# Kernel tuning notes

Hardware: AMD Instinct MI355X
Metric: run time of the kernel (lower is better)

## Reference

```python
import jax, jax.numpy as jnp
import numpy as np


def setup_inputs() -> dict:
    key = jax.random.key(0)
    ks = jax.random.split(key, 8)
    B, T, D, S, E, V = 8, 64, 1024, 32, 16, 50257
    SCALE = 0.02  # keep dot-products in a sane range for softmax
    return {
        "decoder_states": jax.random.normal(ks[0], (B, T, D), jnp.float32),
        "scene_memory": jax.random.normal(ks[1], (B, S, D), jnp.float32),
        "embedding_weight": jax.random.normal(ks[2], (V, D), jnp.float32) * SCALE,
        "ent_ids": jax.random.randint(ks[3], (B, S, E), 0, V, jnp.int32),
        "Wq": jax.random.normal(ks[4], (D, D), jnp.float32) * SCALE,
        "bq": jnp.zeros((D,), jnp.float32),
        "Wk": jax.random.normal(ks[5], (D, D), jnp.float32) * SCALE,
        "bk": jnp.zeros((D,), jnp.float32),
        "Wp": jax.random.normal(ks[6], (2 * D, 1), jnp.float32) * SCALE,
        "bp": jnp.full((1,), 3.0, jnp.float32),  # nn.init.constant_(bias, 3.0)
    }


def reference(decoder_states, scene_memory, embedding_weight, ent_ids,
              Wq, bq, Wk, bk, Wp, bp):
    B, T, D = decoder_states.shape
    S = scene_memory.shape[1]
    V = embedding_weight.shape[0]

    # scene-level attention
    q = decoder_states @ Wq + bq            # [B,T,D]
    k = scene_memory @ Wk + bk              # [B,S,D]
    scores = jnp.einsum('btd,bsd->bts', q, k) / jnp.sqrt(jnp.float32(D))
    scene_attn = jax.nn.softmax(scores, axis=-1)          # [B,T,S]
    context = jnp.einsum('bts,bsd->btd', scene_attn, scene_memory)

    # hard p_gen gate
    gate_in = jnp.concatenate([decoder_states, context], axis=-1)  # [B,T,2D]
    p_gen = jax.nn.sigmoid((gate_in @ Wp + bp - 0.5) * 10.0)       # [B,T,1]

    # entity salience per scene, scattered into V-sized tensor
    dec_last = decoder_states[:, -1, :]                   # [B,D]
    ent_embs = embedding_weight[ent_ids]                  # [B,S,E,D] gather
    salience = jax.nn.softmax(
        jnp.einsum('bd,bsed->bse', dec_last, ent_embs), axis=-1)  # [B,S,E]
    bi = jnp.arange(B)[:, None, None]
    si = jnp.arange(S)[None, :, None]
    scene_to_token = jnp.zeros((B, S, V), decoder_states.dtype)
    scene_to_token = scene_to_token.at[bi, si, ent_ids].set(salience)

    pointer_probs = jnp.einsum('bts,bsv->btv', scene_attn, scene_to_token)
    return p_gen, pointer_probs
```

## Files before the change

kernel.cpp:

```cpp
#include <hip/hip_runtime.h>
#include <math.h>

#define BB 8
#define TT 64
#define DD 1024
#define SS 32
#define EE 16
#define VV 50257
#define BT (BB*TT)
#define BS (BB*SS)

__global__ __launch_bounds__(256) void gemm_qk(
    const float* __restrict__ dec, const float* __restrict__ scene,
    const float* __restrict__ Wq, const float* __restrict__ bq,
    const float* __restrict__ Wk, const float* __restrict__ bk,
    float* __restrict__ q, float* __restrict__ k)
{
    __shared__ __align__(16) float As[16][68];
    __shared__ __align__(16) float Bs[16][68];
    const int bn = blockIdx.x;
    const int bm = blockIdx.y;
    const bool isq = (bm < 8);
    const float* X   = isq ? dec : scene;
    const float* W   = isq ? Wq  : Wk;
    const float* bia = isq ? bq  : bk;
    float*       Y   = isq ? q   : k;
    const int row0 = (isq ? bm : bm - 8) * 64;
    const int col0 = bn * 64;
    const int tid = threadIdx.x;
    const int tx = tid & 15, ty = tid >> 4;

    float acc[4][4] = {};
    for (int k0 = 0; k0 < DD; k0 += 16) {
        {
            const int m  = tid >> 2;
            const int kc = (tid & 3) * 4;
            const float4 x4 = *(const float4*)&X[(size_t)(row0 + m) * DD + k0 + kc];
            As[kc + 0][m] = x4.x; As[kc + 1][m] = x4.y;
            As[kc + 2][m] = x4.z; As[kc + 3][m] = x4.w;
        }
        {
            const int kk = tid >> 4;
            const int nc = (tid & 15) * 4;
            *(float4*)&Bs[kk][nc] = *(const float4*)&W[(size_t)(k0 + kk) * DD + col0 + nc];
        }
        __syncthreads();
        #pragma unroll
        for (int kk = 0; kk < 16; ++kk) {
            float a[4], b[4];
            #pragma unroll
            for (int i = 0; i < 4; ++i) a[i] = As[kk][ty * 4 + i];
            #pragma unroll
            for (int j = 0; j < 4; ++j) b[j] = Bs[kk][tx * 4 + j];
            #pragma unroll
            for (int i = 0; i < 4; ++i)
                #pragma unroll
                for (int j = 0; j < 4; ++j)
                    acc[i][j] += a[i] * b[j];
        }
        __syncthreads();
    }
    #pragma unroll
    for (int i = 0; i < 4; ++i) {
        const int r = row0 + ty * 4 + i;
        #pragma unroll
        for (int j = 0; j < 4; ++j) {
            const int c = col0 + tx * 4 + j;
            Y[(size_t)r * DD + c] = acc[i][j] + bia[c];
        }
    }
}

__global__ __launch_bounds__(64) void dots_kernel(
    const float* __restrict__ dec, const float* __restrict__ scene,
    const float* __restrict__ Wp, float* __restrict__ dw, float* __restrict__ mw)
{
    const int b = blockIdx.x;
    const int lane = threadIdx.x;
    const float* x; const float* wp; float* out;
    if (b < BT) { x = dec   + (size_t)b * DD;        wp = Wp;      out = dw + b; }
    else        { x = scene + (size_t)(b - BT) * DD; wp = Wp + DD; out = mw + (b - BT); }
    float s = 0.f;
    #pragma unroll 4
    for (int i = lane; i < DD; i += 64) s += x[i] * wp[i];
    for (int off = 32; off; off >>= 1) s += __shfl_down(s, off);
    if (lane == 0) *out = s;
}

__global__ __launch_bounds__(256) void attn_kernel(
    const float* __restrict__ qm, const float* __restrict__ km,
    const float* __restrict__ dwv, const float* __restrict__ mwv,
    const float* __restrict__ bp,
    float* __restrict__ attn_out, float* __restrict__ pgen_out)
{
    __shared__ __align__(16) float qs[DD];
    __shared__ float sc[SS];
    const int bt = blockIdx.x;
    const int b  = bt / TT;
    const int tid = threadIdx.x;
    for (int i = tid; i < DD; i += 256) qs[i] = qm[(size_t)bt * DD + i];
    __syncthreads();
    const int w = tid >> 6, lane = tid & 63;
    for (int j = 0; j < 8; ++j) {
        const int s = w * 8 + j;
        const float* kr = km + (size_t)(b * SS + s) * DD;
        float acc = 0.f;
        #pragma unroll
        for (int i = 0; i < 16; ++i) acc += qs[lane + 64 * i] * kr[lane + 64 * i];
        for (int off = 32; off; off >>= 1) acc += __shfl_down(acc, off);
        if (lane == 0) sc[s] = acc * 0.03125f;
    }
    __syncthreads();
    if (tid < 64) {
        float v = (lane < SS) ? sc[lane] : -INFINITY;
        float m = v;
        for (int off = 32; off; off >>= 1) m = fmaxf(m, __shfl_xor(m, off));
        float e = (lane < SS) ? __expf(v - m) : 0.f;
        float sum = e;
        for (int off = 32; off; off >>= 1) sum += __shfl_xor(sum, off);
        const float a = e / sum;
        float g = (lane < SS) ? a * mwv[b * SS + lane] : 0.f;
        for (int off = 32; off; off >>= 1) g += __shfl_xor(g, off);
        if (lane < SS) attn_out[bt * SS + lane] = a;
        if (lane == 0) {
            const float z = dwv[bt] + g + bp[0] - 0.5f;
            pgen_out[bt] = 1.0f / (1.0f + __expf(-10.0f * z));
        }
    }
}

__global__ __launch_bounds__(256) void sal_kernel(
    const float* __restrict__ dec, const float* __restrict__ emb,
    const int* __restrict__ ids, float* __restrict__ sal)
{
    __shared__ __align__(16) float ds[DD];
    __shared__ float logit[EE];
    __shared__ int lid[EE];
    const int bs = blockIdx.x;
    const int b  = bs / SS;
    const int tid = threadIdx.x;
    const float* dl = dec + (size_t)(b * TT + (TT - 1)) * DD;
    for (int i = tid; i < DD; i += 256) ds[i] = dl[i];
    if (tid < EE) lid[tid] = ids[bs * EE + tid];
    __syncthreads();
    const int w = tid >> 6, lane = tid & 63;
    for (int j = 0; j < 4; ++j) {
        const int e = w * 4 + j;
        const float* er = emb + (size_t)lid[e] * DD;
        float acc = 0.f;
        #pragma unroll
        for (int i = 0; i < 16; ++i) acc += ds[lane + 64 * i] * er[lane + 64 * i];
        for (int off = 32; off; off >>= 1) acc += __shfl_down(acc, off);
        if (lane == 0) logit[e] = acc;
    }
    __syncthreads();
    if (tid == 0) {
        float m = -INFINITY;
        for (int e = 0; e < EE; ++e) m = fmaxf(m, logit[e]);
        float ex[EE]; float sum = 0.f;
        for (int e = 0; e < EE; ++e) { ex[e] = __expf(logit[e] - m); sum += ex[e]; }
        const float inv = 1.0f / sum;
        for (int e = 0; e < EE; ++e) {
            bool dup = false;
            for (int e2 = e + 1; e2 < EE; ++e2)
                if (lid[e2] == lid[e]) { dup = true; break; }
            sal[bs * EE + e] = dup ? 0.f : ex[e] * inv;
        }
    }
}

__global__ __launch_bounds__(256) void pp_kernel(
    const float* __restrict__ attn, const float* __restrict__ sal,
    const int* __restrict__ ids, float* __restrict__ pp)
{
    __shared__ float at[SS];
    const int bt = blockIdx.x;
    const int b  = bt / TT;
    const int tid = threadIdx.x;
    if (tid < SS) at[tid] = attn[bt * SS + tid];
    float* row = pp + (size_t)bt * VV;
    for (int i = tid; i < VV; i += 256) row[i] = 0.f;
    __syncthreads();
    for (int i = tid; i < SS * EE; i += 256) {
        const int s = i >> 4, e = i & 15;
        const float v = at[s] * sal[(b * SS + s) * EE + e];
        atomicAdd(&row[ids[(b * SS + s) * EE + e]], v);
    }
}

extern "C" void kernel_launch(void* const* d_in, const int* in_sizes, int n_in,
                              void* d_out, int out_size, void* d_ws, size_t ws_size,
                              hipStream_t stream) {
    (void)in_sizes; (void)n_in; (void)ws_size; (void)out_size;
    const float* dec   = (const float*)d_in[0];
    const float* scene = (const float*)d_in[1];
    const float* emb   = (const float*)d_in[2];
    const int*   ids   = (const int*)  d_in[3];
    const float* Wq    = (const float*)d_in[4];
    const float* bq    = (const float*)d_in[5];
    const float* Wk    = (const float*)d_in[6];
    const float* bk    = (const float*)d_in[7];
    const float* Wp    = (const float*)d_in[8];
    const float* bp    = (const float*)d_in[9];
    float* out = (float*)d_out;
    float* ws  = (float*)d_ws;

    float* q    = ws;
    float* k    = q    + 512 * 1024;
    float* attn = k    + 256 * 1024;
    float* sal  = attn + 512 * 32;
    float* dw   = sal  + 256 * 16;
    float* mw   = dw   + 512;

    gemm_qk<<<dim3(16, 12), 256, 0, stream>>>(dec, scene, Wq, bq, Wk, bk, q, k);
    dots_kernel<<<768, 64, 0, stream>>>(dec, scene, Wp, dw, mw);
    attn_kernel<<<512, 256, 0, stream>>>(q, k, dw, mw, bp, attn, out);
    sal_kernel<<<256, 256, 0, stream>>>(dec, emb, ids, sal);
    pp_kernel<<<512, 256, 0, stream>>>(attn, sal, ids, out + 512);
}
```

Baseline: 389.7 us.

## Switch Q/K projection to bf16 MFMA and fuse small kernels

```diff
diff --git a/kernel.cpp b/kernel.cpp
--- a/kernel.cpp
+++ b/kernel.cpp
@@ -1,4 +1,5 @@
 #include <hip/hip_runtime.h>
+#include <hip/hip_bf16.h>
 #include <math.h>
 
 #define BB 8
@@ -10,161 +11,212 @@
 #define BT (BB*TT)
 #define BS (BB*SS)
 
-__global__ __launch_bounds__(256) void gemm_qk(
+typedef __attribute__((ext_vector_type(8))) short short8;
+typedef __attribute__((ext_vector_type(4))) float floatx4;
+
+static __device__ inline unsigned short f2bf(float x) {
+    __hip_bfloat16 h = __float2bfloat16(x);
+    union { __hip_bfloat16 h; unsigned short u; } cv; cv.h = h;
+    return cv.u;
+}
+
+static __device__ inline void gl_lds16(const void* g, void* l) {
+    __builtin_amdgcn_global_load_lds(
+        (const __attribute__((address_space(1))) void*)g,
+        (__attribute__((address_space(3))) void*)l, 16, 0, 0);
+}
+
+__global__ __launch_bounds__(256) void prep_kernel(
     const float* __restrict__ dec, const float* __restrict__ scene,
-    const float* __restrict__ Wq, const float* __restrict__ bq,
-    const float* __restrict__ Wk, const float* __restrict__ bk,
-    float* __restrict__ q, float* __restrict__ k)
-{
-    __shared__ __align__(16) float As[16][68];
-    __shared__ __align__(16) float Bs[16][68];
-    const int bn = blockIdx.x;
-    const int bm = blockIdx.y;
-    const bool isq = (bm < 8);
-    const float* X   = isq ? dec : scene;
-    const float* W   = isq ? Wq  : Wk;
-    const float* bia = isq ? bq  : bk;
-    float*       Y   = isq ? q   : k;
-    const int row0 = (isq ? bm : bm - 8) * 64;
-    const int col0 = bn * 64;
+    const float* __restrict__ Wq, const float* __restrict__ Wk,
+    const float* __restrict__ Wp,
+    unsigned short* __restrict__ Xb, unsigned short* __restrict__ Wt,
+    float* __restrict__ dw, float* __restrict__ mw)
+{
+    __shared__ float tile[64][65];
+    const int bid = blockIdx.x;
+    const int t = threadIdx.x;
+    if (bid < 768) {
+        const int row = bid;
+        const float* src = (row < BT) ? dec + (size_t)row * DD
+                                      : scene + (size_t)(row - BT) * DD;
+        const float4 v = *(const float4*)&src[t * 4];
+        ushort4 u;
+        u.x = f2bf(v.x); u.y = f2bf(v.y); u.z = f2bf(v.z); u.w = f2bf(v.w);
+        *(ushort4*)&Xb[(size_t)row * DD + t * 4] = u;
+    } else if (bid < 1280) {
+        const int tb = bid - 768;
+        const int sel = tb >> 8;
+        const int tt8 = tb & 255;
+        const int k0 = (tt8 >> 4) * 64, n0 = (tt8 & 15) * 64;
+        const float* Wsrc = sel ? Wk : Wq;
+        const int c4 = (t & 15) * 4;
+        #pragma unroll
+        for (int i = 0; i < 4; ++i) {
+            const int r = (t >> 4) + 16 * i;
+            const float4 v = *(const float4*)&Wsrc[(size_t)(k0 + r) * DD + n0 + c4];
+            tile[r][c4 + 0] = v.x; tile[r][c4 + 1] = v.y;
+            tile[r][c4 + 2] = v.z; tile[r][c4 + 3] = v.w;
+        }
+        __syncthreads();
+        #pragma unroll
+        for (int i = 0; i < 4; ++i) {
+            const int n = (t >> 4) + 16 * i;
+            ushort4 u;
+            u.x = f2bf(tile[c4 + 0][n]); u.y = f2bf(tile[c4 + 1][n]);
+            u.z = f2bf(tile[c4 + 2][n]); u.w = f2bf(tile[c4 + 3][n]);
+            *(ushort4*)&Wt[(size_t)sel * DD * DD + (size_t)(n0 + n) * DD + k0 + c4] = u;
+        }
+    } else {
+        const int di = bid - 1280;
+        const float* x; const float* wp; float* outp;
+        if (di < BT) { x = dec   + (size_t)di * DD;        wp = Wp;      outp = dw + di; }
+        else         { x = scene + (size_t)(di - BT) * DD; wp = Wp + DD; outp = mw + (di - BT); }
+        float s = 0.f;
+        #pragma unroll
+        for (int i = 0; i < 4; ++i) s += x[t + 256 * i] * wp[t + 256 * i];
+        for (int off = 32; off; off >>= 1) s += __shfl_down(s, off);
+        if ((t & 63) == 0) tile[0][t >> 6] = s;
+        __syncthreads();
+        if (t == 0) *outp = tile[0][0] + tile[0][1] + tile[0][2] + tile[0][3];
+    }
+}
+
+__global__ __launch_bounds__(128) void gemm_mfma(
+    const unsigned short* __restrict__ Xb, const unsigned short* __restrict__ Wt,
+    const float* __restrict__ bq, const float* __restrict__ bk,
+    float* __restrict__ qo, float* __restrict__ ko)
+{
+    __shared__ unsigned short As[32 * 32];
+    __shared__ unsigned short Bs[64 * 32];
+    const int bid = blockIdx.x;
+    const int bm = bid >> 4;
+    const int bn = bid & 15;
+    const int m0 = bm * 32, n0 = bn * 64;
+    const bool isq = (bm < 16);
+    const unsigned short* Wsel = Wt + (isq ? 0 : (size_t)DD * DD);
     const int tid = threadIdx.x;
-    const int tx = tid & 15, ty = tid >> 4;
-
-    float acc[4][4] = {};
-    for (int k0 = 0; k0 < DD; k0 += 16) {
-        {
-            const int m  = tid >> 2;
-            const int kc = (tid & 3) * 4;
-            const float4 x4 = *(const float4*)&X[(size_t)(row0 + m) * DD + k0 + kc];
-            As[kc + 0][m] = x4.x; As[kc + 1][m] = x4.y;
-            As[kc + 2][m] = x4.z; As[kc + 3][m] = x4.w;
-        }
-        {
-            const int kk = tid >> 4;
-            const int nc = (tid & 15) * 4;
-            *(float4*)&Bs[kk][nc] = *(const float4*)&W[(size_t)(k0 + kk) * DD + col0 + nc];
-        }
-        __syncthreads();
-        #pragma unroll
-        for (int kk = 0; kk < 16; ++kk) {
-            float a[4], b[4];
-            #pragma unroll
-            for (int i = 0; i < 4; ++i) a[i] = As[kk][ty * 4 + i];
-            #pragma unroll
-            for (int j = 0; j < 4; ++j) b[j] = Bs[kk][tx * 4 + j];
-            #pragma unroll
-            for (int i = 0; i < 4; ++i)
-                #pragma unroll
-                for (int j = 0; j < 4; ++j)
-                    acc[i][j] += a[i] * b[j];
-        }
-        __syncthreads();
+    const int w = tid >> 6, l = tid & 63;
+
+    const int arow = 16 * w + (l >> 2);
+    const int kb8  = (l & 3) * 8;
+    floatx4 acc[4] = {{0.f,0.f,0.f,0.f},{0.f,0.f,0.f,0.f},
+                      {0.f,0.f,0.f,0.f},{0.f,0.f,0.f,0.f}};
+
+    for (int k0 = 0; k0 < DD; k0 += 32) {
+        __syncthreads();
+        gl_lds16(&Xb[(size_t)(m0 + arow) * DD + k0 + kb8], &As[w * 512]);
+        #pragma unroll
+        for (int i = 0; i < 2; ++i) {
+            const int brow = 32 * w + 16 * i + (l >> 2);
+            gl_lds16(&Wsel[(size_t)(n0 + brow) * DD + k0 + kb8],
+                     &Bs[w * 1024 + i * 512]);
+        }
+        __syncthreads();
+        const short8 a = *(const short8*)&As[(16 * w + (l & 15)) * 32 + (l >> 4) * 8];
+        #pragma unroll
+        for (int j = 0; j < 4; ++j) {
+            const short8 b = *(const short8*)&Bs[(16 * j + (l & 15)) * 32 + (l >> 4) * 8];
+            acc[j] = __builtin_amdgcn_mfma_f32_16x16x32_bf16(a, b, acc[j], 0, 0, 0);
+        }
     }
     #pragma unroll
-    for (int i = 0; i < 4; ++i) {
-        const int r = row0 + ty * 4 + i;
-        #pragma unroll
-        for (int j = 0; j < 4; ++j) {
-            const int c = col0 + tx * 4 + j;
-            Y[(size_t)r * DD + c] = acc[i][j] + bia[c];
-        }
-    }
-}
-
-__global__ __launch_bounds__(64) void dots_kernel(
-    const float* __restrict__ dec, const float* __restrict__ scene,
-    const float* __restrict__ Wp, float* __restrict__ dw, float* __restrict__ mw)
-{
-    const int b = blockIdx.x;
-    const int lane = threadIdx.x;
-    const float* x; const float* wp; float* out;
-    if (b < BT) { x = dec   + (size_t)b * DD;        wp = Wp;      out = dw + b; }
-    else        { x = scene + (size_t)(b - BT) * DD; wp = Wp + DD; out = mw + (b - BT); }
-    float s = 0.f;
-    #pragma unroll 4
-    for (int i = lane; i < DD; i += 64) s += x[i] * wp[i];
-    for (int off = 32; off; off >>= 1) s += __shfl_down(s, off);
-    if (lane == 0) *out = s;
-}
-
-__global__ __launch_bounds__(256) void attn_kernel(
+    for (int j = 0; j < 4; ++j) {
+        const int gcol = n0 + 16 * j + (l & 15);
+        const float bias = isq ? bq[gcol] : bk[gcol];
+        #pragma unroll
+        for (int r = 0; r < 4; ++r) {
+            const int grow = m0 + 16 * w + (l >> 4) * 4 + r;
+            const float val = acc[j][r] + bias;
+            if (isq) qo[(size_t)grow * DD + gcol] = val;
+            else     ko[(size_t)(grow - BT) * DD + gcol] = val;
+        }
+    }
+}
+
+__global__ __launch_bounds__(256) void attn_sal_kernel(
     const float* __restrict__ qm, const float* __restrict__ km,
+    const float* __restrict__ dec, const float* __restrict__ emb,
+    const int* __restrict__ ids,
     const float* __restrict__ dwv, const float* __restrict__ mwv,
     const float* __restrict__ bp,
-    float* __restrict__ attn_out, float* __restrict__ pgen_out)
+    float* __restrict__ attn_out, float* __restrict__ pgen_out,
+    float* __restrict__ sal_out)
 {
     __shared__ __align__(16) float qs[DD];
     __shared__ float sc[SS];
-    const int bt = blockIdx.x;
-    const int b  = bt / TT;
+    __shared__ int lid[EE];
     const int tid = threadIdx.x;
-    for (int i = tid; i < DD; i += 256) qs[i] = qm[(size_t)bt * DD + i];
-    __syncthreads();
     const int w = tid >> 6, lane = tid & 63;
-    for (int j = 0; j < 8; ++j) {
-        const int s = w * 8 + j;
-        const float* kr = km + (size_t)(b * SS + s) * DD;
-        float acc = 0.f;
-        #pragma unroll
-        for (int i = 0; i < 16; ++i) acc += qs[lane + 64 * i] * kr[lane + 64 * i];
-        for (int off = 32; off; off >>= 1) acc += __shfl_down(acc, off);
-        if (lane == 0) sc[s] = acc * 0.03125f;
-    }
-    __syncthreads();
-    if (tid < 64) {
-        float v = (lane < SS) ? sc[lane] : -INFINITY;
-        float m = v;
-        for (int off = 32; off; off >>= 1) m = fmaxf(m, __shfl_xor(m, off));
-        float e = (lane < SS) ? __expf(v - m) : 0.f;
-        float sum = e;
-        for (int off = 32; off; off >>= 1) sum += __shfl_xor(sum, off);
-        const float a = e / sum;
-        float g = (lane < SS) ? a * mwv[b * SS + lane] : 0.f;
-        for (int off = 32; off; off >>= 1) g += __shfl_xor(g, off);
-        if (lane < SS) attn_out[bt * SS + lane] = a;
-        if (lane == 0) {
-            const float z = dwv[bt] + g + bp[0] - 0.5f;
-            pgen_out[bt] = 1.0f / (1.0f + __expf(-10.0f * z));
-        }
-    }
-}
-
-__global__ __launch_bounds__(256) void sal_kernel(
-    const float* __restrict__ dec, const float* __restrict__ emb,
-    const int* __restrict__ ids, float* __restrict__ sal)
-{
-    __shared__ __align__(16) float ds[DD];
-    __shared__ float logit[EE];
-    __shared__ int lid[EE];
-    const int bs = blockIdx.x;
-    const int b  = bs / SS;
-    const int tid = threadIdx.x;
-    const float* dl = dec + (size_t)(b * TT + (TT - 1)) * DD;
-    for (int i = tid; i < DD; i += 256) ds[i] = dl[i];
-    if (tid < EE) lid[tid] = ids[bs * EE + tid];
-    __syncthreads();
-    const int w = tid >> 6, lane = tid & 63;
-    for (int j = 0; j < 4; ++j) {
-        const int e = w * 4 + j;
-        const float* er = emb + (size_t)lid[e] * DD;
-        float acc = 0.f;
-        #pragma unroll
-        for (int i = 0; i < 16; ++i) acc += ds[lane + 64 * i] * er[lane + 64 * i];
-        for (int off = 32; off; off >>= 1) acc += __shfl_down(acc, off);
-        if (lane == 0) logit[e] = acc;
-    }
-    __syncthreads();
-    if (tid == 0) {
-        float m = -INFINITY;
-        for (int e = 0; e < EE; ++e) m = fmaxf(m, logit[e]);
-        float ex[EE]; float sum = 0.f;
-        for (int e = 0; e < EE; ++e) { ex[e] = __expf(logit[e] - m); sum += ex[e]; }
-        const float inv = 1.0f / sum;
-        for (int e = 0; e < EE; ++e) {
-            bool dup = false;
-            for (int e2 = e + 1; e2 < EE; ++e2)
-                if (lid[e2] == lid[e]) { dup = true; break; }
-            sal[bs * EE + e] = dup ? 0.f : ex[e] * inv;
+
+    if (blockIdx.x < BT) {
+        const int bt = blockIdx.x;
+        const int b  = bt / TT;
+        *(float4*)&qs[tid * 4] = *(const float4*)&qm[(size_t)bt * DD + tid * 4];
+        __syncthreads();
+        for (int j = 0; j < 8; ++j) {
+            const int s = w * 8 + j;
+            const float* kr = km + (size_t)(b * SS + s) * DD;
+            float accv = 0.f;
+            #pragma unroll
+            for (int i = 0; i < 4; ++i) {
+                const float4 qv = *(const float4*)&qs[4 * lane + 256 * i];
+                const float4 kv = *(const float4*)&kr[4 * lane + 256 * i];
+                accv += qv.x * kv.x + qv.y * kv.y + qv.z * kv.z + qv.w * kv.w;
+            }
+            for (int off = 32; off; off >>= 1) accv += __shfl_down(accv, off);
+            if (lane == 0) sc[s] = accv * 0.03125f;
+        }
+        __syncthreads();
+        if (tid < 64) {
+            float v = (lane < SS) ? sc[lane] : -INFINITY;
+            float m = v;
+            for (int off = 32; off; off >>= 1) m = fmaxf(m, __shfl_xor(m, off));
+            float e = (lane < SS) ? __expf(v - m) : 0.f;
+            float sum = e;
+            for (int off = 32; off; off >>= 1) sum += __shfl_xor(sum, off);
+            const float a = e / sum;
+            float g = (lane < SS) ? a * mwv[b * SS + lane] : 0.f;
+            for (int off = 32; off; off >>= 1) g += __shfl_xor(g, off);
+            if (lane < SS) attn_out[bt * SS + lane] = a;
+            if (lane == 0) {
+                const float z = dwv[bt] + g + bp[0] - 0.5f;
+                pgen_out[bt] = 1.0f / (1.0f + __expf(-10.0f * z));
+            }
+        }
+    } else {
+        const int bs = blockIdx.x - BT;
+        const int b  = bs / SS;
+        const float* dl = dec + (size_t)(b * TT + (TT - 1)) * DD;
+        *(float4*)&qs[tid * 4] = *(const float4*)&dl[tid * 4];
+        if (tid < EE) lid[tid] = ids[bs * EE + tid];
+        __syncthreads();
+        for (int j = 0; j < 4; ++j) {
+            const int e = w * 4 + j;
+            const float* er = emb + (size_t)lid[e] * DD;
+            float accv = 0.f;
+            #pragma unroll
+            for (int i = 0; i < 4; ++i) {
+                const float4 dv = *(const float4*)&qs[4 * lane + 256 * i];
+                const float4 ev = *(const float4*)&er[4 * lane + 256 * i];
+                accv += dv.x * ev.x + dv.y * ev.y + dv.z * ev.z + dv.w * ev.w;
+            }
+            for (int off = 32; off; off >>= 1) accv += __shfl_down(accv, off);
+            if (lane == 0) sc[e] = accv;
+        }
+        __syncthreads();
+        if (tid == 0) {
+            float m = -INFINITY;
+            for (int e = 0; e < EE; ++e) m = fmaxf(m, sc[e]);
+            float ex[EE]; float sum = 0.f;
+            for (int e = 0; e < EE; ++e) { ex[e] = __expf(sc[e] - m); sum += ex[e]; }
+            const float inv = 1.0f / sum;
+            for (int e = 0; e < EE; ++e) {
+                bool dup = false;
+                for (int e2 = e + 1; e2 < EE; ++e2)
+                    if (lid[e2] == lid[e]) { dup = true; break; }
+                sal_out[bs * EE + e] = dup ? 0.f : ex[e] * inv;
+            }
         }
     }
 }
@@ -179,7 +231,14 @@
     const int tid = threadIdx.x;
     if (tid < SS) at[tid] = attn[bt * SS + tid];
     float* row = pp + (size_t)bt * VV;
-    for (int i = tid; i < VV; i += 256) row[i] = 0.f;
+    const int h = (4 - (bt & 3)) & 3;
+    if (tid < h) row[tid] = 0.f;
+    const int nv = (VV - h) >> 2;
+    float4* rv = (float4*)(row + h);
+    const float4 z4 = make_float4(0.f, 0.f, 0.f, 0.f);
+    for (int i = tid; i < nv; i += 256) rv[i] = z4;
+    const int tail = (VV - h) & 3;
+    if (tid < tail) row[h + 4 * nv + tid] = 0.f;
     __syncthreads();
     for (int i = tid; i < SS * EE; i += 256) {
         const int s = i >> 4, e = i & 15;
@@ -206,15 +265,17 @@
     float* ws  = (float*)d_ws;
 
     float* q    = ws;
-    float* k    = q    + 512 * 1024;
-    float* attn = k    + 256 * 1024;
+    float* kbuf = q    + 512 * 1024;
+    float* attn = kbuf + 256 * 1024;
     float* sal  = attn + 512 * 32;
     float* dw   = sal  + 256 * 16;
     float* mw   = dw   + 512;
-
-    gemm_qk<<<dim3(16, 12), 256, 0, stream>>>(dec, scene, Wq, bq, Wk, bk, q, k);
-    dots_kernel<<<768, 64, 0, stream>>>(dec, scene, Wp, dw, mw);
-    attn_kernel<<<512, 256, 0, stream>>>(q, k, dw, mw, bp, attn, out);
-    sal_kernel<<<256, 256, 0, stream>>>(dec, emb, ids, sal);
+    unsigned short* Xb = (unsigned short*)(mw + 256);
+    unsigned short* Wt = Xb + 768 * 1024;
+
+    prep_kernel<<<2048, 256, 0, stream>>>(dec, scene, Wq, Wk, Wp, Xb, Wt, dw, mw);
+    gemm_mfma<<<384, 128, 0, stream>>>(Xb, Wt, bq, bk, q, kbuf);
+    attn_sal_kernel<<<768, 256, 0, stream>>>(q, kbuf, dec, emb, ids, dw, mw, bp,
+                                             attn, out, sal);
     pp_kernel<<<512, 256, 0, stream>>>(attn, sal, ids, out + 512);
 }
```

Result: faster. 327.4 us, median of 2 (-16.0%).
